# Kernel optimization log

Hardware: AMD Instinct MI355X
Metric: run time of the kernel (lower is better)

## Reference

```python
import math
import jax, jax.numpy as jnp
import numpy as np

N = 100000
E_RAND = 800000
IN_F, HID, OUT_F, HEADS = 128, 64, 64, 4
NOISE_SCALE = 1.0 * math.sqrt(2.0 * math.log(1.25 / 0.05))  # dp_rate=1, eps=1, del=0.05


def setup_inputs() -> dict:
    key = jax.random.key(0)
    ks = jax.random.split(key, 12)
    x = jax.random.normal(ks[0], (N, IN_F), dtype=jnp.float32)
    src_r = jax.random.randint(ks[1], (E_RAND,), 0, N, dtype=jnp.int32)
    dst_r = jax.random.randint(ks[2], (E_RAND,), 0, N, dtype=jnp.int32)
    loops = jnp.arange(N, dtype=jnp.int32)  # add_self_loop
    src = jnp.concatenate([src_r, loops])
    dst = jnp.concatenate([dst_r, loops])
    # layer 0: GATConv(in=128, out=64, heads=4)
    s0 = 1.0 / math.sqrt(IN_F)
    W0 = jax.random.normal(ks[3], (IN_F, HEADS * HID), dtype=jnp.float32) * s0
    al0 = jax.random.normal(ks[4], (HEADS, HID), dtype=jnp.float32) * 0.1
    ar0 = jax.random.normal(ks[5], (HEADS, HID), dtype=jnp.float32) * 0.1
    b0 = jnp.zeros((HEADS * HID,), dtype=jnp.float32)
    # layer 1: GATConv(in=256, out=64, heads=1)
    s1 = 1.0 / math.sqrt(HEADS * HID)
    W1 = jax.random.normal(ks[6], (HEADS * HID, OUT_F), dtype=jnp.float32) * s1
    al1 = jax.random.normal(ks[7], (1, OUT_F), dtype=jnp.float32) * 0.1
    ar1 = jax.random.normal(ks[8], (1, OUT_F), dtype=jnp.float32) * 0.1
    b1 = jnp.zeros((OUT_F,), dtype=jnp.float32)
    # DP gaussian noise added after first GAT layer (torch.normal(0,1,x.shape))
    noise = jax.random.normal(ks[9], (N, HEADS * HID), dtype=jnp.float32)
    return {"x": x, "src": src, "dst": dst, "W0": W0, "al0": al0, "ar0": ar0,
            "b0": b0, "W1": W1, "al1": al1, "ar1": ar1, "b1": b1, "noise": noise}


def gat_conv(x, src, dst, W, al, ar, b, apply_act):
    """DGL GATConv: per-edge attention, edge softmax over dst, scatter-sum."""
    H, D = al.shape
    h = (x @ W).reshape(-1, H, D)                      # [N,H,D]
    el = jnp.sum(h * al, axis=-1)                      # [N,H]
    er = jnp.sum(h * ar, axis=-1)                      # [N,H]
    e = jax.nn.leaky_relu(el[src] + er[dst], 0.2)      # [E,H]
    emax = jax.ops.segment_max(e, dst, num_segments=N) # [N,H]
    a = jnp.exp(e - emax[dst])
    denom = jax.ops.segment_sum(a, dst, num_segments=N)
    alpha = a / denom[dst]                             # [E,H] edge softmax
    msg = h[src] * alpha[:, :, None]                   # [E,H,D]
    out = jax.ops.segment_sum(msg, dst, num_segments=N) + b.reshape(1, H, D)
    if apply_act:
        out = jax.nn.leaky_relu(out, 0.01)             # F.leaky_relu default slope
    return out.reshape(-1, H * D)                      # flatten(1)


def reference(x, src, dst, W0, al0, ar0, b0, W1, al1, ar1, b1, noise):
    h = gat_conv(x, src, dst, W0, al0, ar0, b0, apply_act=True)   # [N, 256]
    h = h + NOISE_SCALE * noise                                   # DP noise after layer 0
    out = gat_conv(h, src, dst, W1, al1, ar1, b1, apply_act=False)  # [N, 64]
    return out
```

## Files before the change

kernel.cpp:

```cpp
#include <hip/hip_runtime.h>
#include <hip/hip_bf16.h>
#include <math.h>

#define IN_F 128
#define HID 64
#define HEADS 4
#define HD0 (HEADS * HID)
#define OUT_F 64
#define NOISE_SCALE 2.5372725354060904f

typedef __bf16 bf16x8 __attribute__((ext_vector_type(8)));
typedef float f32x4 __attribute__((ext_vector_type(4)));

__device__ __forceinline__ float bf2f(unsigned short u) {
    return __uint_as_float(((unsigned)u) << 16);
}
__device__ __forceinline__ unsigned short f2bf(float f) {
    unsigned u = __float_as_uint(f);
    u = u + 0x7fffu + ((u >> 16) & 1u);
    return (unsigned short)(u >> 16);
}

__device__ __forceinline__ void acc8(float* acc, const uint4& u, float wt) {
    acc[0] += wt * __uint_as_float(u.x << 16);
    acc[1] += wt * __uint_as_float(u.x & 0xffff0000u);
    acc[2] += wt * __uint_as_float(u.y << 16);
    acc[3] += wt * __uint_as_float(u.y & 0xffff0000u);
    acc[4] += wt * __uint_as_float(u.z << 16);
    acc[5] += wt * __uint_as_float(u.z & 0xffff0000u);
    acc[6] += wt * __uint_as_float(u.w << 16);
    acc[7] += wt * __uint_as_float(u.w & 0xffff0000u);
}

__global__ __launch_bounds__(256) void cast_bf16_kernel(
    const float* __restrict__ in, unsigned short* __restrict__ out, size_t n8,
    int* __restrict__ deg, int N) {
    size_t i = (size_t)blockIdx.x * 256 + threadIdx.x;
    if (i < (size_t)N) deg[i] = 0;
    if (i >= n8) return;
    const float4 a = ((const float4*)in)[i * 2];
    const float4 b = ((const float4*)in)[i * 2 + 1];
    ushort4 o0, o1;
    o0.x = f2bf(a.x); o0.y = f2bf(a.y); o0.z = f2bf(a.z); o0.w = f2bf(a.w);
    o1.x = f2bf(b.x); o1.y = f2bf(b.y); o1.z = f2bf(b.z); o1.w = f2bf(b.w);
    ((ushort4*)out)[i * 2] = o0;
    ((ushort4*)out)[i * 2 + 1] = o1;
}

__global__ __launch_bounds__(256) void tcast2_kernel(
    const float* __restrict__ W0, unsigned short* __restrict__ W0t,
    const float* __restrict__ W1, unsigned short* __restrict__ W1t) {
    int i = blockIdx.x * 256 + threadIdx.x;
    if (i < IN_F * HD0) {
        int n = i / IN_F, k = i % IN_F;
        W0t[i] = f2bf(W0[(size_t)k * HD0 + n]);
    } else {
        int j = i - IN_F * HD0;
        if (j < HD0 * OUT_F) {
            int n = j / HD0, k = j % HD0;
            W1t[j] = f2bf(W1[(size_t)k * OUT_F + n]);
        }
    }
}

template <int K, int H>
__global__ __launch_bounds__(256) void gemm_fused_kernel(
    const unsigned short* __restrict__ A, const unsigned short* __restrict__ Bt,
    unsigned short* __restrict__ C, const float* __restrict__ al,
    const float* __restrict__ ar, float* __restrict__ el,
    float* __restrict__ er, int M, int NC) {
    constexpr int BSTR = K + 8;
    constexpr int ASTR = 40;
    __shared__ __align__(16) unsigned short Bs[64 * BSTR];
    __shared__ __align__(16) unsigned short As[128 * ASTR];
    const int tid = threadIdx.x;
    const int lane = tid & 63, w = tid >> 6;
    const int row0 = blockIdx.y * 128;
    const int n0 = blockIdx.x * 64;
    for (int i = tid; i < 64 * (K / 8); i += 256) {
        int n = i / (K / 8), kc = i % (K / 8);
        *(uint4*)(Bs + n * BSTR + kc * 8) =
            *(const uint4*)(Bt + (size_t)(n0 + n) * K + kc * 8);
    }
    f32x4 acc[2][4] = {};
    const int q = lane >> 4, c = lane & 15;
    const int r_st = tid >> 1, hh = tid & 1;
    for (int k0 = 0; k0 < K; k0 += 32) {
        int gr = row0 + r_st;
        uint4 av0 = make_uint4(0, 0, 0, 0), av1 = make_uint4(0, 0, 0, 0);
        if (gr < M) {
            const unsigned short* ap = A + (size_t)gr * K + k0 + hh * 16;
            av0 = *(const uint4*)(ap);
            av1 = *(const uint4*)(ap + 8);
        }
        __syncthreads();
        *(uint4*)(As + r_st * ASTR + hh * 16) = av0;
        *(uint4*)(As + r_st * ASTR + hh * 16 + 8) = av1;
        __syncthreads();
        bf16x8 af[2], bfr[4];
        af[0] = *(const bf16x8*)(As + (w * 32 + c) * ASTR + q * 8);
        af[1] = *(const bf16x8*)(As + (w * 32 + 16 + c) * ASTR + q * 8);
#pragma unroll
        for (int nt = 0; nt < 4; ++nt)
            bfr[nt] = *(const bf16x8*)(Bs + (nt * 16 + c) * BSTR + k0 + q * 8);
#pragma unroll
        for (int mt = 0; mt < 2; ++mt)
#pragma unroll
            for (int nt = 0; nt < 4; ++nt)
                acc[mt][nt] = __builtin_amdgcn_mfma_f32_16x16x32_bf16(
                    af[mt], bfr[nt], acc[mt][nt], 0, 0, 0);
    }
    float alv[4], arv[4];
#pragma unroll
    for (int nt = 0; nt < 4; ++nt) {
        alv[nt] = al[n0 + nt * 16 + c];
        arv[nt] = ar[n0 + nt * 16 + c];
    }
    const int head = n0 >> 6;
#pragma unroll
    for (int mt = 0; mt < 2; ++mt) {
#pragma unroll
        for (int r = 0; r < 4; ++r) {
            int grow = row0 + w * 32 + mt * 16 + q * 4 + r;
            bool ok = grow < M;
            float elp = 0.f, erp = 0.f;
#pragma unroll
            for (int nt = 0; nt < 4; ++nt) {
                float v = acc[mt][nt][r];
                elp += v * alv[nt];
                erp += v * arv[nt];
                if (ok) C[(size_t)grow * NC + n0 + nt * 16 + c] = f2bf(v);
            }
#pragma unroll
            for (int o = 8; o > 0; o >>= 1) {
                elp += __shfl_down(elp, o, 16);
                erp += __shfl_down(erp, o, 16);
            }
            if (c == 0 && ok) {
                el[(size_t)grow * H + head] = elp;
                er[(size_t)grow * H + head] = erp;
            }
        }
    }
}

__global__ __launch_bounds__(256) void degree_kernel(
    const int* __restrict__ dst, int* __restrict__ deg, int E) {
    int e = blockIdx.x * 256 + threadIdx.x;
    if (e < E) atomicAdd(&deg[dst[e]], 1);
}

__global__ __launch_bounds__(256) void scan_block_kernel(
    const int* __restrict__ deg, int* __restrict__ off,
    int* __restrict__ bsum, int N) {
    __shared__ int s[256];
    int i = blockIdx.x * 256 + threadIdx.x;
    int v = (i < N) ? deg[i] : 0;
    s[threadIdx.x] = v;
    __syncthreads();
    for (int d = 1; d < 256; d <<= 1) {
        int t = (threadIdx.x >= d) ? s[threadIdx.x - d] : 0;
        __syncthreads();
        s[threadIdx.x] += t;
        __syncthreads();
    }
    if (i < N) off[i] = s[threadIdx.x] - v;
    if (threadIdx.x == 255) bsum[blockIdx.x] = s[255];
}

__global__ __launch_bounds__(512) void scan_partials_kernel(int* __restrict__ bsum, int nb) {
    __shared__ int s[512];
    int v = (threadIdx.x < nb) ? bsum[threadIdx.x] : 0;
    s[threadIdx.x] = v;
    __syncthreads();
    for (int d = 1; d < 512; d <<= 1) {
        int t = (threadIdx.x >= d) ? s[threadIdx.x - d] : 0;
        __syncthreads();
        s[threadIdx.x] += t;
        __syncthreads();
    }
    if (threadIdx.x < nb) bsum[threadIdx.x] = s[threadIdx.x] - v;
}

__global__ __launch_bounds__(256) void add_offsets_kernel(
    int* __restrict__ off, int* __restrict__ cur,
    const int* __restrict__ bsum, int N, int E) {
    int i = blockIdx.x * 256 + threadIdx.x;
    if (i < N) {
        int v = off[i] + bsum[blockIdx.x];
        off[i] = v;
        cur[i] = v;
    }
    if (i == 0) off[N] = E;
}

__global__ __launch_bounds__(256) void fill_csr_kernel(
    const int* __restrict__ src, const int* __restrict__ dst,
    int* __restrict__ cur, int* __restrict__ csr_src, int E) {
    int e = blockIdx.x * 256 + threadIdx.x;
    if (e >= E) return;
    int d = dst[e];
    int pos = atomicAdd(&cur[d], 1);
    csr_src[pos] = src[e];
}

__global__ __launch_bounds__(256) void agg0_kernel(
    const int* __restrict__ off, const int* __restrict__ csr_src,
    const unsigned short* __restrict__ h,
    const float* __restrict__ el,
    const float* __restrict__ er,
    const float* __restrict__ b0, const float* __restrict__ noise,
    unsigned short* __restrict__ out, int N) {
    int gt = blockIdx.x * 256 + threadIdx.x;
    int n = gt >> 5;
    if (n >= N) return;
    const int lane = gt & 31;
    const int hd = lane >> 3;
    const int f0 = lane << 3;
    const float ern = er[(size_t)n * 4 + hd];
    const int beg = off[n];
    const int last = off[n + 1] - 1;
    float acc[8] = {0.f, 0.f, 0.f, 0.f, 0.f, 0.f, 0.f, 0.f};
    float l = 0.f;
    for (int p = beg; p <= last; p += 4) {
        int i1 = p + 1, i2 = p + 2, i3 = p + 3;
        const bool v1 = i1 <= last, v2 = i2 <= last, v3 = i3 <= last;
        i1 = v1 ? i1 : last;
        i2 = v2 ? i2 : last;
        i3 = v3 ? i3 : last;
        const int s0 = csr_src[p],  s1 = csr_src[i1];
        const int s2 = csr_src[i2], s3 = csr_src[i3];
        float e0 = el[(size_t)s0 * 4 + hd] + ern;
        float e1 = el[(size_t)s1 * 4 + hd] + ern;
        float e2 = el[(size_t)s2 * 4 + hd] + ern;
        float e3 = el[(size_t)s3 * 4 + hd] + ern;
        const uint4 u0 = *(const uint4*)(h + (size_t)s0 * HD0 + f0);
        const uint4 u1 = *(const uint4*)(h + (size_t)s1 * HD0 + f0);
        const uint4 u2 = *(const uint4*)(h + (size_t)s2 * HD0 + f0);
        const uint4 u3 = *(const uint4*)(h + (size_t)s3 * HD0 + f0);
        e0 = e0 > 0.f ? e0 : 0.2f * e0;
        e1 = e1 > 0.f ? e1 : 0.2f * e1;
        e2 = e2 > 0.f ? e2 : 0.2f * e2;
        e3 = e3 > 0.f ? e3 : 0.2f * e3;
        const float w0 = __expf(e0);
        const float w1 = v1 ? __expf(e1) : 0.f;
        const float w2 = v2 ? __expf(e2) : 0.f;
        const float w3 = v3 ? __expf(e3) : 0.f;
        acc8(acc, u0, w0);
        acc8(acc, u1, w1);
        acc8(acc, u2, w2);
        acc8(acc, u3, w3);
        l += (w0 + w1) + (w2 + w3);
    }
    const float rd = 1.f / l;
    const float4 ba = *(const float4*)(b0 + f0);
    const float4 bb = *(const float4*)(b0 + f0 + 4);
    const float4 na = *(const float4*)(noise + (size_t)n * HD0 + f0);
    const float4 nb = *(const float4*)(noise + (size_t)n * HD0 + f0 + 4);
    float o[8];
    o[0] = acc[0] * rd + ba.x;
    o[1] = acc[1] * rd + ba.y;
    o[2] = acc[2] * rd + ba.z;
    o[3] = acc[3] * rd + ba.w;
    o[4] = acc[4] * rd + bb.x;
    o[5] = acc[5] * rd + bb.y;
    o[6] = acc[6] * rd + bb.z;
    o[7] = acc[7] * rd + bb.w;
#pragma unroll
    for (int j = 0; j < 8; ++j) o[j] = o[j] > 0.f ? o[j] : 0.01f * o[j];
    o[0] += NOISE_SCALE * na.x;
    o[1] += NOISE_SCALE * na.y;
    o[2] += NOISE_SCALE * na.z;
    o[3] += NOISE_SCALE * na.w;
    o[4] += NOISE_SCALE * nb.x;
    o[5] += NOISE_SCALE * nb.y;
    o[6] += NOISE_SCALE * nb.z;
    o[7] += NOISE_SCALE * nb.w;
    uint4 ov;
    ov.x = (unsigned)f2bf(o[0]) | ((unsigned)f2bf(o[1]) << 16);
    ov.y = (unsigned)f2bf(o[2]) | ((unsigned)f2bf(o[3]) << 16);
    ov.z = (unsigned)f2bf(o[4]) | ((unsigned)f2bf(o[5]) << 16);
    ov.w = (unsigned)f2bf(o[6]) | ((unsigned)f2bf(o[7]) << 16);
    *(uint4*)(out + (size_t)n * HD0 + f0) = ov;
}

__global__ __launch_bounds__(256) void agg1_kernel(
    const int* __restrict__ off, const int* __restrict__ csr_src,
    const unsigned short* __restrict__ h,
    const float* __restrict__ el,
    const float* __restrict__ er,
    const float* __restrict__ b1, float* __restrict__ out, int N) {
    int gt = blockIdx.x * 256 + threadIdx.x;
    int n = gt >> 4;
    if (n >= N) return;
    const int lane = gt & 15;
    const int f0 = lane << 2;
    const float ern = er[n];
    const int beg = off[n];
    const int last = off[n + 1] - 1;
    float a0 = 0.f, a1 = 0.f, a2 = 0.f, a3 = 0.f, l = 0.f;
    for (int p = beg; p <= last; p += 4) {
        int i1 = p + 1, i2 = p + 2, i3 = p + 3;
        const bool v1 = i1 <= last, v2 = i2 <= last, v3 = i3 <= last;
        i1 = v1 ? i1 : last;
        i2 = v2 ? i2 : last;
        i3 = v3 ? i3 : last;
        const int s0 = csr_src[p],  s1 = csr_src[i1];
        const int s2 = csr_src[i2], s3 = csr_src[i3];
        float e0 = el[s0] + ern;
        float e1 = el[s1] + ern;
        float e2 = el[s2] + ern;
        float e3 = el[s3] + ern;
        const ushort4 u0 = *(const ushort4*)(h + (size_t)s0 * 64 + f0);
        const ushort4 u1 = *(const ushort4*)(h + (size_t)s1 * 64 + f0);
        const ushort4 u2 = *(const ushort4*)(h + (size_t)s2 * 64 + f0);
        const ushort4 u3 = *(const ushort4*)(h + (size_t)s3 * 64 + f0);
        e0 = e0 > 0.f ? e0 : 0.2f * e0;
        e1 = e1 > 0.f ? e1 : 0.2f * e1;
        e2 = e2 > 0.f ? e2 : 0.2f * e2;
        e3 = e3 > 0.f ? e3 : 0.2f * e3;
        const float w0 = __expf(e0);
        const float w1 = v1 ? __expf(e1) : 0.f;
        const float w2 = v2 ? __expf(e2) : 0.f;
        const float w3 = v3 ? __expf(e3) : 0.f;
        a0 += w0 * bf2f(u0.x) + w1 * bf2f(u1.x) + w2 * bf2f(u2.x) + w3 * bf2f(u3.x);
        a1 += w0 * bf2f(u0.y) + w1 * bf2f(u1.y) + w2 * bf2f(u2.y) + w3 * bf2f(u3.y);
        a2 += w0 * bf2f(u0.z) + w1 * bf2f(u1.z) + w2 * bf2f(u2.z) + w3 * bf2f(u3.z);
        a3 += w0 * bf2f(u0.w) + w1 * bf2f(u1.w) + w2 * bf2f(u2.w) + w3 * bf2f(u3.w);
        l += (w0 + w1) + (w2 + w3);
    }
    const float rd = 1.f / l;
    const float4 bv = *(const float4*)(b1 + f0);
    float4 o;
    o.x = a0 * rd + bv.x;
    o.y = a1 * rd + bv.y;
    o.z = a2 * rd + bv.z;
    o.w = a3 * rd + bv.w;
    *(float4*)(out + (size_t)n * 64 + f0) = o;
}

extern "C" void kernel_launch(void* const* d_in, const int* in_sizes, int n_in,
                              void* d_out, int out_size, void* d_ws, size_t ws_size,
                              hipStream_t stream) {
    const float* x     = (const float*)d_in[0];
    const int*   src   = (const int*)d_in[1];
    const int*   dst   = (const int*)d_in[2];
    const float* W0    = (const float*)d_in[3];
    const float* al0   = (const float*)d_in[4];
    const float* ar0   = (const float*)d_in[5];
    const float* b0    = (const float*)d_in[6];
    const float* W1    = (const float*)d_in[7];
    const float* al1   = (const float*)d_in[8];
    const float* ar1   = (const float*)d_in[9];
    const float* b1    = (const float*)d_in[10];
    const float* noise = (const float*)d_in[11];

    const int N = in_sizes[0] / IN_F;
    const int E = in_sizes[1];
    const int NB = (N + 255) / 256;

    char* p = (char*)d_ws;
    unsigned short* x_bf   = (unsigned short*)p; p += (size_t)N * IN_F * 2;
    unsigned short* h0     = (unsigned short*)p; p += (size_t)N * HD0 * 2;
    unsigned short* agg0b  = (unsigned short*)p; p += (size_t)N * HD0 * 2;
    unsigned short* h1     = (unsigned short*)p; p += (size_t)N * OUT_F * 2;
    unsigned short* W0t    = (unsigned short*)p; p += (size_t)IN_F * HD0 * 2;
    unsigned short* W1t    = (unsigned short*)p; p += (size_t)HD0 * OUT_F * 2;
    float* el     = (float*)p; p += (size_t)N * HEADS * 4;
    float* er     = (float*)p; p += (size_t)N * HEADS * 4;
    int* deg    = (int*)p; p += (size_t)N * 4;
    int* cur    = (int*)p; p += (size_t)N * 4;
    int* off    = (int*)p; p += ((size_t)N + 4) * 4;
    int* bsum   = (int*)p; p += 512 * 4;
    int* csr_src= (int*)p; p += (size_t)E * 4;

    {
        size_t n8 = (size_t)N * IN_F / 8;
        cast_bf16_kernel<<<(unsigned)((n8 + 255) / 256), 256, 0, stream>>>(
            x, x_bf, n8, deg, N);
    }
    tcast2_kernel<<<(IN_F * HD0 + HD0 * OUT_F + 255) / 256, 256, 0, stream>>>(
        W0, W0t, W1, W1t);

    degree_kernel<<<(E + 255) / 256, 256, 0, stream>>>(dst, deg, E);
    scan_block_kernel<<<NB, 256, 0, stream>>>(deg, off, bsum, N);
    scan_partials_kernel<<<1, 512, 0, stream>>>(bsum, NB);
    add_offsets_kernel<<<NB, 256, 0, stream>>>(off, cur, bsum, N, E);
    fill_csr_kernel<<<(E + 255) / 256, 256, 0, stream>>>(src, dst, cur, csr_src, E);

    const int MB = (N + 127) / 128;

    {
        dim3 grid(HD0 / 64, MB);
        gemm_fused_kernel<IN_F, HEADS><<<grid, 256, 0, stream>>>(
            x_bf, W0t, h0, al0, ar0, el, er, N, HD0);
    }
    agg0_kernel<<<(unsigned)(((size_t)N * 32 + 255) / 256), 256, 0, stream>>>(
        off, csr_src, h0, el, er, b0, noise, agg0b, N);

    {
        dim3 grid(OUT_F / 64, MB);
        gemm_fused_kernel<HD0, 1><<<grid, 256, 0, stream>>>(
            agg0b, W1t, h1, al1, ar1, el, er, N, OUT_F);
    }
    agg1_kernel<<<(unsigned)(((size_t)N * 16 + 255) / 256), 256, 0, stream>>>(
        off, csr_src, h1, el, er, b1, (float*)d_out, N);
}
```

Measured before the change: 435.2 us.

## Merge prep kernels, widen layer-0 GEMM tile, unroll edge gathers by eight

Folds the x cast and the two weight transpose-casts into a single prep launch. The layer-0 GEMM now covers 128 output columns per block (two heads), so each A tile is loaded half as often. Both aggregation kernels now process eight edges per iteration and issue all the gathers before the math, giving more memory-level parallelism. The costs are higher register pressure and more LDS in the GEMM, and more wasted loads on the tail of low-degree nodes.

```diff
diff --git a/kernel.cpp b/kernel.cpp
--- a/kernel.cpp
+++ b/kernel.cpp
@@ -32,30 +32,29 @@
     acc[7] += wt * __uint_as_float(u.w & 0xffff0000u);
 }
 
-__global__ __launch_bounds__(256) void cast_bf16_kernel(
+__global__ __launch_bounds__(256) void prep_kernel(
     const float* __restrict__ in, unsigned short* __restrict__ out, size_t n8,
-    int* __restrict__ deg, int N) {
-    size_t i = (size_t)blockIdx.x * 256 + threadIdx.x;
-    if (i < (size_t)N) deg[i] = 0;
-    if (i >= n8) return;
-    const float4 a = ((const float4*)in)[i * 2];
-    const float4 b = ((const float4*)in)[i * 2 + 1];
-    ushort4 o0, o1;
-    o0.x = f2bf(a.x); o0.y = f2bf(a.y); o0.z = f2bf(a.z); o0.w = f2bf(a.w);
-    o1.x = f2bf(b.x); o1.y = f2bf(b.y); o1.z = f2bf(b.z); o1.w = f2bf(b.w);
-    ((ushort4*)out)[i * 2] = o0;
-    ((ushort4*)out)[i * 2 + 1] = o1;
-}
-
-__global__ __launch_bounds__(256) void tcast2_kernel(
+    int* __restrict__ deg, int N, int nb_cast,
     const float* __restrict__ W0, unsigned short* __restrict__ W0t,
     const float* __restrict__ W1, unsigned short* __restrict__ W1t) {
-    int i = blockIdx.x * 256 + threadIdx.x;
-    if (i < IN_F * HD0) {
+    const int b = blockIdx.x;
+    if (b < nb_cast) {
+        size_t i = (size_t)b * 256 + threadIdx.x;
+        if (i < (size_t)N) deg[i] = 0;
+        if (i >= n8) return;
+        const float4 a = ((const float4*)in)[i * 2];
+        const float4 c = ((const float4*)in)[i * 2 + 1];
+        ushort4 o0, o1;
+        o0.x = f2bf(a.x); o0.y = f2bf(a.y); o0.z = f2bf(a.z); o0.w = f2bf(a.w);
+        o1.x = f2bf(c.x); o1.y = f2bf(c.y); o1.z = f2bf(c.z); o1.w = f2bf(c.w);
+        ((ushort4*)out)[i * 2] = o0;
+        ((ushort4*)out)[i * 2 + 1] = o1;
+    } else if (b < nb_cast + (IN_F * HD0) / 256) {
+        int i = (b - nb_cast) * 256 + threadIdx.x;
         int n = i / IN_F, k = i % IN_F;
         W0t[i] = f2bf(W0[(size_t)k * HD0 + n]);
     } else {
-        int j = i - IN_F * HD0;
+        int j = (b - nb_cast - (IN_F * HD0) / 256) * 256 + threadIdx.x;
         if (j < HD0 * OUT_F) {
             int n = j / HD0, k = j % HD0;
             W1t[j] = f2bf(W1[(size_t)k * OUT_F + n]);
@@ -63,7 +62,7 @@
     }
 }
 
-template <int K, int H>
+template <int K, int H, int NT>
 __global__ __launch_bounds__(256) void gemm_fused_kernel(
     const unsigned short* __restrict__ A, const unsigned short* __restrict__ Bt,
     unsigned short* __restrict__ C, const float* __restrict__ al,
@@ -71,18 +70,19 @@
     float* __restrict__ er, int M, int NC) {
     constexpr int BSTR = K + 8;
     constexpr int ASTR = 40;
-    __shared__ __align__(16) unsigned short Bs[64 * BSTR];
+    constexpr int NROWS = 64 * NT;
+    __shared__ __align__(16) unsigned short Bs[NROWS * BSTR];
     __shared__ __align__(16) unsigned short As[128 * ASTR];
     const int tid = threadIdx.x;
     const int lane = tid & 63, w = tid >> 6;
     const int row0 = blockIdx.y * 128;
-    const int n0 = blockIdx.x * 64;
-    for (int i = tid; i < 64 * (K / 8); i += 256) {
+    const int n0 = blockIdx.x * NROWS;
+    for (int i = tid; i < NROWS * (K / 8); i += 256) {
         int n = i / (K / 8), kc = i % (K / 8);
         *(uint4*)(Bs + n * BSTR + kc * 8) =
             *(const uint4*)(Bt + (size_t)(n0 + n) * K + kc * 8);
     }
-    f32x4 acc[2][4] = {};
+    f32x4 acc[2][4 * NT] = {};
     const int q = lane >> 4, c = lane & 15;
     const int r_st = tid >> 1, hh = tid & 1;
     for (int k0 = 0; k0 < K; k0 += 32) {
@@ -97,48 +97,52 @@
         *(uint4*)(As + r_st * ASTR + hh * 16) = av0;
         *(uint4*)(As + r_st * ASTR + hh * 16 + 8) = av1;
         __syncthreads();
-        bf16x8 af[2], bfr[4];
+        bf16x8 af[2], bfr[4 * NT];
         af[0] = *(const bf16x8*)(As + (w * 32 + c) * ASTR + q * 8);
         af[1] = *(const bf16x8*)(As + (w * 32 + 16 + c) * ASTR + q * 8);
 #pragma unroll
-        for (int nt = 0; nt < 4; ++nt)
+        for (int nt = 0; nt < 4 * NT; ++nt)
             bfr[nt] = *(const bf16x8*)(Bs + (nt * 16 + c) * BSTR + k0 + q * 8);
 #pragma unroll
         for (int mt = 0; mt < 2; ++mt)
 #pragma unroll
-            for (int nt = 0; nt < 4; ++nt)
+            for (int nt = 0; nt < 4 * NT; ++nt)
                 acc[mt][nt] = __builtin_amdgcn_mfma_f32_16x16x32_bf16(
                     af[mt], bfr[nt], acc[mt][nt], 0, 0, 0);
     }
-    float alv[4], arv[4];
-#pragma unroll
-    for (int nt = 0; nt < 4; ++nt) {
+    float alv[4 * NT], arv[4 * NT];
+#pragma unroll
+    for (int nt = 0; nt < 4 * NT; ++nt) {
         alv[nt] = al[n0 + nt * 16 + c];
         arv[nt] = ar[n0 + nt * 16 + c];
     }
-    const int head = n0 >> 6;
+    const int headbase = n0 >> 6;
 #pragma unroll
     for (int mt = 0; mt < 2; ++mt) {
 #pragma unroll
         for (int r = 0; r < 4; ++r) {
             int grow = row0 + w * 32 + mt * 16 + q * 4 + r;
             bool ok = grow < M;
-            float elp = 0.f, erp = 0.f;
-#pragma unroll
-            for (int nt = 0; nt < 4; ++nt) {
-                float v = acc[mt][nt][r];
-                elp += v * alv[nt];
-                erp += v * arv[nt];
-                if (ok) C[(size_t)grow * NC + n0 + nt * 16 + c] = f2bf(v);
-            }
-#pragma unroll
-            for (int o = 8; o > 0; o >>= 1) {
-                elp += __shfl_down(elp, o, 16);
-                erp += __shfl_down(erp, o, 16);
-            }
-            if (c == 0 && ok) {
-                el[(size_t)grow * H + head] = elp;
-                er[(size_t)grow * H + head] = erp;
+#pragma unroll
+            for (int g = 0; g < NT; ++g) {
+                float elp = 0.f, erp = 0.f;
+#pragma unroll
+                for (int t = 0; t < 4; ++t) {
+                    int nt = g * 4 + t;
+                    float v = acc[mt][nt][r];
+                    elp += v * alv[nt];
+                    erp += v * arv[nt];
+                    if (ok) C[(size_t)grow * NC + n0 + nt * 16 + c] = f2bf(v);
+                }
+#pragma unroll
+                for (int o = 8; o > 0; o >>= 1) {
+                    elp += __shfl_down(elp, o, 16);
+                    erp += __shfl_down(erp, o, 16);
+                }
+                if (c == 0 && ok) {
+                    el[(size_t)grow * H + headbase + g] = elp;
+                    er[(size_t)grow * H + headbase + g] = erp;
+                }
             }
         }
     }
@@ -222,35 +226,29 @@
     const int last = off[n + 1] - 1;
     float acc[8] = {0.f, 0.f, 0.f, 0.f, 0.f, 0.f, 0.f, 0.f};
     float l = 0.f;
-    for (int p = beg; p <= last; p += 4) {
-        int i1 = p + 1, i2 = p + 2, i3 = p + 3;
-        const bool v1 = i1 <= last, v2 = i2 <= last, v3 = i3 <= last;
-        i1 = v1 ? i1 : last;
-        i2 = v2 ? i2 : last;
-        i3 = v3 ? i3 : last;
-        const int s0 = csr_src[p],  s1 = csr_src[i1];
-        const int s2 = csr_src[i2], s3 = csr_src[i3];
-        float e0 = el[(size_t)s0 * 4 + hd] + ern;
-        float e1 = el[(size_t)s1 * 4 + hd] + ern;
-        float e2 = el[(size_t)s2 * 4 + hd] + ern;
-        float e3 = el[(size_t)s3 * 4 + hd] + ern;
-        const uint4 u0 = *(const uint4*)(h + (size_t)s0 * HD0 + f0);
-        const uint4 u1 = *(const uint4*)(h + (size_t)s1 * HD0 + f0);
-        const uint4 u2 = *(const uint4*)(h + (size_t)s2 * HD0 + f0);
-        const uint4 u3 = *(const uint4*)(h + (size_t)s3 * HD0 + f0);
-        e0 = e0 > 0.f ? e0 : 0.2f * e0;
-        e1 = e1 > 0.f ? e1 : 0.2f * e1;
-        e2 = e2 > 0.f ? e2 : 0.2f * e2;
-        e3 = e3 > 0.f ? e3 : 0.2f * e3;
-        const float w0 = __expf(e0);
-        const float w1 = v1 ? __expf(e1) : 0.f;
-        const float w2 = v2 ? __expf(e2) : 0.f;
-        const float w3 = v3 ? __expf(e3) : 0.f;
-        acc8(acc, u0, w0);
-        acc8(acc, u1, w1);
-        acc8(acc, u2, w2);
-        acc8(acc, u3, w3);
-        l += (w0 + w1) + (w2 + w3);
+    for (int p = beg; p <= last; p += 8) {
+        int idx[8]; bool v[8]; int s[8]; float e[8]; uint4 u[8]; float wt[8];
+#pragma unroll
+        for (int j = 0; j < 8; ++j) {
+            int ij = p + j;
+            v[j] = ij <= last;
+            idx[j] = v[j] ? ij : last;
+        }
+#pragma unroll
+        for (int j = 0; j < 8; ++j) s[j] = csr_src[idx[j]];
+#pragma unroll
+        for (int j = 0; j < 8; ++j) e[j] = el[(size_t)s[j] * 4 + hd];
+#pragma unroll
+        for (int j = 0; j < 8; ++j) u[j] = *(const uint4*)(h + (size_t)s[j] * HD0 + f0);
+#pragma unroll
+        for (int j = 0; j < 8; ++j) {
+            float t = e[j] + ern;
+            t = t > 0.f ? t : 0.2f * t;
+            wt[j] = v[j] ? __expf(t) : 0.f;
+            l += wt[j];
+        }
+#pragma unroll
+        for (int j = 0; j < 8; ++j) acc8(acc, u[j], wt[j]);
     }
     const float rd = 1.f / l;
     const float4 ba = *(const float4*)(b0 + f0);
@@ -299,35 +297,34 @@
     const int beg = off[n];
     const int last = off[n + 1] - 1;
     float a0 = 0.f, a1 = 0.f, a2 = 0.f, a3 = 0.f, l = 0.f;
-    for (int p = beg; p <= last; p += 4) {
-        int i1 = p + 1, i2 = p + 2, i3 = p + 3;
-        const bool v1 = i1 <= last, v2 = i2 <= last, v3 = i3 <= last;
-        i1 = v1 ? i1 : last;
-        i2 = v2 ? i2 : last;
-        i3 = v3 ? i3 : last;
-        const int s0 = csr_src[p],  s1 = csr_src[i1];
-        const int s2 = csr_src[i2], s3 = csr_src[i3];
-        float e0 = el[s0] + ern;
-        float e1 = el[s1] + ern;
-        float e2 = el[s2] + ern;
-        float e3 = el[s3] + ern;
-        const ushort4 u0 = *(const ushort4*)(h + (size_t)s0 * 64 + f0);
-        const ushort4 u1 = *(const ushort4*)(h + (size_t)s1 * 64 + f0);
-        const ushort4 u2 = *(const ushort4*)(h + (size_t)s2 * 64 + f0);
-        const ushort4 u3 = *(const ushort4*)(h + (size_t)s3 * 64 + f0);
-        e0 = e0 > 0.f ? e0 : 0.2f * e0;
-        e1 = e1 > 0.f ? e1 : 0.2f * e1;
-        e2 = e2 > 0.f ? e2 : 0.2f * e2;
-        e3 = e3 > 0.f ? e3 : 0.2f * e3;
-        const float w0 = __expf(e0);
-        const float w1 = v1 ? __expf(e1) : 0.f;
-        const float w2 = v2 ? __expf(e2) : 0.f;
-        const float w3 = v3 ? __expf(e3) : 0.f;
-        a0 += w0 * bf2f(u0.x) + w1 * bf2f(u1.x) + w2 * bf2f(u2.x) + w3 * bf2f(u3.x);
-        a1 += w0 * bf2f(u0.y) + w1 * bf2f(u1.y) + w2 * bf2f(u2.y) + w3 * bf2f(u3.y);
-        a2 += w0 * bf2f(u0.z) + w1 * bf2f(u1.z) + w2 * bf2f(u2.z) + w3 * bf2f(u3.z);
-        a3 += w0 * bf2f(u0.w) + w1 * bf2f(u1.w) + w2 * bf2f(u2.w) + w3 * bf2f(u3.w);
-        l += (w0 + w1) + (w2 + w3);
+    for (int p = beg; p <= last; p += 8) {
+        int idx[8]; bool v[8]; int s[8]; float e[8]; ushort4 u[8]; float wt[8];
+#pragma unroll
+        for (int j = 0; j < 8; ++j) {
+            int ij = p + j;
+            v[j] = ij <= last;
+            idx[j] = v[j] ? ij : last;
+        }
+#pragma unroll
+        for (int j = 0; j < 8; ++j) s[j] = csr_src[idx[j]];
+#pragma unroll
+        for (int j = 0; j < 8; ++j) e[j] = el[s[j]];
+#pragma unroll
+        for (int j = 0; j < 8; ++j) u[j] = *(const ushort4*)(h + (size_t)s[j] * 64 + f0);
+#pragma unroll
+        for (int j = 0; j < 8; ++j) {
+            float t = e[j] + ern;
+            t = t > 0.f ? t : 0.2f * t;
+            wt[j] = v[j] ? __expf(t) : 0.f;
+            l += wt[j];
+        }
+#pragma unroll
+        for (int j = 0; j < 8; ++j) {
+            a0 += wt[j] * bf2f(u[j].x);
+            a1 += wt[j] * bf2f(u[j].y);
+            a2 += wt[j] * bf2f(u[j].z);
+            a3 += wt[j] * bf2f(u[j].w);
+        }
     }
     const float rd = 1.f / l;
     const float4 bv = *(const float4*)(b1 + f0);
@@ -376,11 +373,12 @@
 
     {
         size_t n8 = (size_t)N * IN_F / 8;
-        cast_bf16_kernel<<<(unsigned)((n8 + 255) / 256), 256, 0, stream>>>(
-            x, x_bf, n8, deg, N);
-    }
-    tcast2_kernel<<<(IN_F * HD0 + HD0 * OUT_F + 255) / 256, 256, 0, stream>>>(
-        W0, W0t, W1, W1t);
+        int nb_cast = (int)((n8 + 255) / 256);
+        int nb_w0 = (IN_F * HD0) / 256;
+        int nb_w1 = (HD0 * OUT_F + 255) / 256;
+        prep_kernel<<<nb_cast + nb_w0 + nb_w1, 256, 0, stream>>>(
+            x, x_bf, n8, deg, N, nb_cast, W0, W0t, W1, W1t);
+    }
 
     degree_kernel<<<(E + 255) / 256, 256, 0, stream>>>(dst, deg, E);
     scan_block_kernel<<<NB, 256, 0, stream>>>(deg, off, bsum, N);
@@ -391,8 +389,8 @@
     const int MB = (N + 127) / 128;
 
     {
-        dim3 grid(HD0 / 64, MB);
-        gemm_fused_kernel<IN_F, HEADS><<<grid, 256, 0, stream>>>(
+        dim3 grid(HD0 / 128, MB);
+        gemm_fused_kernel<IN_F, HEADS, 2><<<grid, 256, 0, stream>>>(
             x_bf, W0t, h0, al0, ar0, el, er, N, HD0);
     }
     agg0_kernel<<<(unsigned)(((size_t)N * 32 + 255) / 256), 256, 0, stream>>>(
@@ -400,7 +398,7 @@
 
     {
         dim3 grid(OUT_F / 64, MB);
-        gemm_fused_kernel<HD0, 1><<<grid, 256, 0, stream>>>(
+        gemm_fused_kernel<HD0, 1, 1><<<grid, 256, 0, stream>>>(
             agg0b, W1t, h1, al1, ar1, el, er, N, OUT_F);
     }
     agg1_kernel<<<(unsigned)(((size_t)N * 16 + 255) / 256), 256, 0, stream>>>(
```

Measured after the change: 441.5 us. No clear change (+1.5%).
